# Performance work log

Hardware: AMD Instinct MI355X
Metric: run time of the kernel (lower is better)

## Reference

```python
import jax, jax.numpy as jnp
import numpy as np

D_MODEL = 1024
NHEAD = 16
HEAD_DIM = D_MODEL // NHEAD
B, L = 4, 8192
LN_EPS = 1e-5


def setup_inputs() -> dict:
    key = jax.random.key(0)
    ks = jax.random.split(key, 8)
    s = 1.0 / np.sqrt(D_MODEL)
    return {
        "x": jax.random.normal(ks[0], (B, L, D_MODEL), dtype=jnp.float32),
        "decay": jax.random.uniform(ks[1], (NHEAD,), dtype=jnp.float32, minval=0.8, maxval=0.999),
        "Wq": jax.random.normal(ks[2], (D_MODEL, D_MODEL), dtype=jnp.float32) * s,
        "Wv": jax.random.normal(ks[3], (D_MODEL, D_MODEL), dtype=jnp.float32) * s,
        "Wg": jax.random.normal(ks[4], (D_MODEL, D_MODEL), dtype=jnp.float32) * s,
        "Wo": jax.random.normal(ks[5], (D_MODEL, D_MODEL), dtype=jnp.float32) * s,
        "ln_gamma": jnp.ones((D_MODEL,), dtype=jnp.float32),
        "ln_beta": jnp.zeros((D_MODEL,), dtype=jnp.float32),
    }


def _decay_scan(v, lam):
    # v: (B, L, H, Dh), lam: (H,). s_t = lam * s_{t-1} + v_t, parallel assoc scan over L.
    a = jnp.broadcast_to(lam[None, None, :, None], v.shape)

    def combine(c1, c2):
        a1, b1 = c1
        a2, b2 = c2
        return a1 * a2, b1 * a2 + b2

    _, state = jax.lax.associative_scan(combine, (a, v), axis=1)
    return state


def _layernorm(y, gamma, beta):
    mu = jnp.mean(y, axis=-1, keepdims=True)
    var = jnp.mean(jnp.square(y - mu), axis=-1, keepdims=True)
    return (y - mu) * jax.lax.rsqrt(var + LN_EPS) * gamma + beta


def reference(x, decay, Wq, Wv, Wg, Wo, ln_gamma, ln_beta):
    Bx, Lx, D = x.shape
    q = (x @ Wq.T).reshape(Bx, Lx, NHEAD, HEAD_DIM)
    v = (x @ Wv.T).reshape(Bx, Lx, NHEAD, HEAD_DIM)
    state = _decay_scan(v, decay)                      # (B, L, H, Dh)
    y = (q * state).reshape(Bx, Lx, D)
    y = _layernorm(y, ln_gamma, ln_beta)
    gate = jax.nn.silu(x @ Wg.T)
    y = y * gate
    return y @ Wo.T
```

## Files before the change

kernel.cpp:

```cpp
#include <hip/hip_runtime.h>
#include <cstdint>
#include <cstddef>

typedef unsigned short u16;
typedef __attribute__((ext_vector_type(4))) float f32x4;
typedef __attribute__((ext_vector_type(8))) short s16x8;
typedef __attribute__((ext_vector_type(4))) short s16x4;

#define D_M   1024
#define KDIM  1024
#define BB    4
#define LL    8192
#define MTOT  (BB*LL)
#define CHK   128
#define NCH   (LL/CHK)
#define LN_EPS 1e-5f

static __device__ __forceinline__ float bf2f(u16 u){
  return __uint_as_float(((unsigned)u)<<16);
}
static __device__ __forceinline__ u16 f2bf(float f){
  unsigned u = __float_as_uint(f);
  u += 0x7fffu + ((u>>16)&1u);
  return (u16)(u>>16);
}

__global__ void conv_f2b_k(const float* __restrict__ src, u16* __restrict__ dst, int n4){
  int i = blockIdx.x*blockDim.x + threadIdx.x;
  int stride = gridDim.x*blockDim.x;
  for (; i < n4; i += stride){
    f32x4 f = ((const f32x4*)src)[i];
    s16x4 o;
    o[0]=(short)f2bf(f[0]); o[1]=(short)f2bf(f[1]);
    o[2]=(short)f2bf(f[2]); o[3]=(short)f2bf(f[3]);
    ((s16x4*)dst)[i] = o;
  }
}

template<int F32OUT>
__global__ __launch_bounds__(256,2) void gemm_bt(
    const u16* __restrict__ A,
    const u16* __restrict__ W0, const u16* __restrict__ W1, const u16* __restrict__ W2,
    void* __restrict__ O0, void* __restrict__ O1, void* __restrict__ O2)
{
  __shared__ __align__(16) u16 As[128*64];
  __shared__ __align__(16) u16 Bs[128*64];
  const int mode = blockIdx.z;
  const u16* W = (mode==0)? W0 : ((mode==1)? W1 : W2);
  void* Ov     = (mode==0)? O0 : ((mode==1)? O1 : O2);

  const int tid  = threadIdx.x;
  const int wave = tid>>6, lane = tid&63;
  const int bm = blockIdx.x*128, bn = blockIdx.y*128;

  size_t ga[4], gb[4];
  int lbase[4];
  #pragma unroll
  for (int it=0; it<4; ++it){
    int c    = it*256 + wave*64 + lane;
    int mch  = c>>3;
    int k16  = (c&7) ^ (mch&7);
    ga[it] = (size_t)(bm + mch)*KDIM + (size_t)k16*8;
    gb[it] = (size_t)(bn + mch)*KDIM + (size_t)k16*8;
    lbase[it] = (it*256 + wave*64)*8;
  }

  const int lr = lane&15, lk = lane>>4;
  const int wm = (wave>>1)*64, wn = (wave&1)*64;
  int a_off[4][2], b_off[4][2];
  #pragma unroll
  for (int mi=0; mi<4; ++mi){
    #pragma unroll
    for (int kp=0; kp<2; ++kp){
      int slot = ((kp*4 + lk) ^ (lr&7));
      a_off[mi][kp] = (wm + mi*16 + lr)*128 + slot*16;
      b_off[mi][kp] = (wn + mi*16 + lr)*128 + slot*16;
    }
  }

  const f32x4 fzero = {0.f,0.f,0.f,0.f};
  f32x4 acc[4][4];
  #pragma unroll
  for (int i=0;i<4;i++)
    #pragma unroll
    for (int j=0;j<4;j++)
      acc[i][j] = fzero;

  const char* Asc = (const char*)As;
  const char* Bsc = (const char*)Bs;

  for (int kt=0; kt<KDIM/64; ++kt){
    if (kt) __syncthreads();
    #pragma unroll
    for (int it=0; it<4; ++it){
      __builtin_amdgcn_global_load_lds(
        (const __attribute__((address_space(1))) void*)(A + ga[it] + (size_t)kt*64),
        (__attribute__((address_space(3))) void*)(As + lbase[it]), 16, 0, 0);
      __builtin_amdgcn_global_load_lds(
        (const __attribute__((address_space(1))) void*)(W + gb[it] + (size_t)kt*64),
        (__attribute__((address_space(3))) void*)(Bs + lbase[it]), 16, 0, 0);
    }
    __syncthreads();
    #pragma unroll
    for (int kp=0; kp<2; ++kp){
      s16x8 af[4], bfr[4];
      #pragma unroll
      for (int mi=0; mi<4; ++mi) af[mi]  = *(const s16x8*)(Asc + a_off[mi][kp]);
      #pragma unroll
      for (int ni=0; ni<4; ++ni) bfr[ni] = *(const s16x8*)(Bsc + b_off[ni][kp]);
      #pragma unroll
      for (int mi=0; mi<4; ++mi)
        #pragma unroll
        for (int ni=0; ni<4; ++ni)
          acc[mi][ni] = __builtin_amdgcn_mfma_f32_16x16x32_bf16(af[mi], bfr[ni], acc[mi][ni], 0,0,0);
    }
  }

  const int r0 = bm + wm + (lane>>4)*4;
  const int c0 = bn + wn + (lane&15);
  if (F32OUT){
    float* O = (float*)Ov;
    #pragma unroll
    for (int mi=0; mi<4; ++mi)
      #pragma unroll
      for (int ni=0; ni<4; ++ni)
        #pragma unroll
        for (int r=0;r<4;r++)
          O[(size_t)(r0 + mi*16 + r)*D_M + (c0 + ni*16)] = acc[mi][ni][r];
  } else {
    u16* O = (u16*)Ov;
    const bool do_silu = (mode==2);
    #pragma unroll
    for (int mi=0; mi<4; ++mi)
      #pragma unroll
      for (int ni=0; ni<4; ++ni)
        #pragma unroll
        for (int r=0;r<4;r++){
          float vv = acc[mi][ni][r];
          if (do_silu) vv = vv / (1.f + __expf(-vv));
          O[(size_t)(r0 + mi*16 + r)*D_M + (c0 + ni*16)] = f2bf(vv);
        }
  }
}

__global__ __launch_bounds__(256) void scan1_k(u16* __restrict__ v, float* __restrict__ E,
                                               const float* __restrict__ decay){
  const int c = blockIdx.x, b = blockIdx.y;
  const int d0 = threadIdx.x*4;
  const float lam = decay[d0>>6];
  float s0=0.f,s1=0.f,s2=0.f,s3=0.f;
  u16* p = v + ((size_t)b*LL + (size_t)c*CHK)*D_M + d0;
  for (int i=0;i<CHK;i++){
    s16x4 x = *(const s16x4*)p;
    s0 = fmaf(s0, lam, bf2f((u16)x[0]));
    s1 = fmaf(s1, lam, bf2f((u16)x[1]));
    s2 = fmaf(s2, lam, bf2f((u16)x[2]));
    s3 = fmaf(s3, lam, bf2f((u16)x[3]));
    s16x4 o;
    o[0]=(short)f2bf(s0); o[1]=(short)f2bf(s1);
    o[2]=(short)f2bf(s2); o[3]=(short)f2bf(s3);
    *(s16x4*)p = o;
    p += D_M;
  }
  f32x4 e = {s0,s1,s2,s3};
  *(f32x4*)(E + ((size_t)(b*NCH + c))*D_M + d0) = e;
}

__global__ void scan2_k(const float* __restrict__ E, float* __restrict__ S,
                        const float* __restrict__ decay){
  const int idx = blockIdx.x*blockDim.x + threadIdx.x;
  if (idx >= BB*(D_M/4)) return;
  const int b  = idx / (D_M/4);
  const int d0 = (idx % (D_M/4))*4;
  const float lam  = decay[d0>>6];
  const float lamT = __expf((float)CHK * __logf(lam));
  f32x4 s = {0.f,0.f,0.f,0.f};
  for (int c=0;c<NCH;c++){
    const size_t o = ((size_t)(b*NCH + c))*D_M + d0;
    f32x4 e = *(const f32x4*)(E + o);
    s = s*lamT + e;
    *(f32x4*)(S + o) = s;
  }
}

__global__ __launch_bounds__(256) void fuse_ln_k(
  const u16* __restrict__ qb, const u16* __restrict__ locb, const u16* __restrict__ gateb,
  const float* __restrict__ S, const float* __restrict__ decay,
  const float* __restrict__ gamma, const float* __restrict__ beta,
  u16* __restrict__ yout)
{
  const int token = blockIdx.x;
  const int b  = token >> 13;
  const int t  = token & (LL-1);
  const int c  = t >> 7;
  const int ii = t & (CHK-1);
  const int tid = threadIdx.x;
  const int d0 = tid*4;
  const float lam = decay[d0>>6];
  const float pw  = __expf((float)(ii+1) * __logf(lam));
  f32x4 carry = {0.f,0.f,0.f,0.f};
  if (c > 0) carry = *(const f32x4*)(S + ((size_t)(b*NCH + (c-1)))*D_M + d0);
  const size_t base = (size_t)token*D_M + d0;
  s16x4 q4 = *(const s16x4*)(qb + base);
  s16x4 l4 = *(const s16x4*)(locb + base);
  float y[4];
  #pragma unroll
  for (int j=0;j<4;j++)
    y[j] = bf2f((u16)q4[j]) * (bf2f((u16)l4[j]) + pw*carry[j]);
  float sum = y[0]+y[1]+y[2]+y[3];
  float sq  = y[0]*y[0]+y[1]*y[1]+y[2]*y[2]+y[3]*y[3];
  #pragma unroll
  for (int off=32; off>0; off>>=1){
    sum += __shfl_down(sum, off);
    sq  += __shfl_down(sq , off);
  }
  __shared__ float red[10];
  const int wave = tid>>6, lane = tid&63;
  if (lane==0){ red[wave] = sum; red[4+wave] = sq; }
  __syncthreads();
  if (tid==0){
    float ts = red[0]+red[1]+red[2]+red[3];
    float tq = red[4]+red[5]+red[6]+red[7];
    float mu  = ts * (1.f/(float)D_M);
    float var = tq * (1.f/(float)D_M) - mu*mu;
    red[8] = mu;
    red[9] = rsqrtf(var + LN_EPS);
  }
  __syncthreads();
  const float mu = red[8], rstd = red[9];
  f32x4 gm = *(const f32x4*)(gamma + d0);
  f32x4 bt = *(const f32x4*)(beta  + d0);
  s16x4 g4 = *(const s16x4*)(gateb + base);
  s16x4 o;
  #pragma unroll
  for (int j=0;j<4;j++){
    float nn = (y[j] - mu)*rstd*gm[j] + bt[j];
    nn *= bf2f((u16)g4[j]);
    o[j] = (short)f2bf(nn);
  }
  *(s16x4*)(yout + base) = o;
}

extern "C" void kernel_launch(void* const* d_in, const int* in_sizes, int n_in,
                              void* d_out, int out_size, void* d_ws, size_t ws_size,
                              hipStream_t stream)
{
  const float* x     = (const float*)d_in[0];
  const float* decay = (const float*)d_in[1];
  const float* Wq    = (const float*)d_in[2];
  const float* Wv    = (const float*)d_in[3];
  const float* Wg    = (const float*)d_in[4];
  const float* Wo    = (const float*)d_in[5];
  const float* gamma = (const float*)d_in[6];
  const float* beta  = (const float*)d_in[7];
  float* out = (float*)d_out;

  char* ws = (char*)d_ws;
  size_t off = 0;
  const size_t XB = (size_t)MTOT*D_M*sizeof(u16);
  const size_t WB = (size_t)D_M*KDIM*sizeof(u16);
  const size_t EB = (size_t)BB*NCH*D_M*sizeof(float);
  u16* xb  = (u16*)(ws+off); off += XB;
  u16* Wqb = (u16*)(ws+off); off += WB;
  u16* Wvb = (u16*)(ws+off); off += WB;
  u16* Wgb = (u16*)(ws+off); off += WB;
  u16* Wob = (u16*)(ws+off); off += WB;
  u16* qb  = (u16*)(ws+off); off += XB;
  u16* vb  = (u16*)(ws+off); off += XB;
  u16* gb  = (u16*)(ws+off); off += XB;
  float* E = (float*)(ws+off); off += EB;
  float* S = (float*)(ws+off); off += EB;

  conv_f2b_k<<<dim3(4096), 256, 0, stream>>>(x,  xb,  MTOT*D_M/4);
  conv_f2b_k<<<dim3(512),  256, 0, stream>>>(Wq, Wqb, D_M*KDIM/4);
  conv_f2b_k<<<dim3(512),  256, 0, stream>>>(Wv, Wvb, D_M*KDIM/4);
  conv_f2b_k<<<dim3(512),  256, 0, stream>>>(Wg, Wgb, D_M*KDIM/4);
  conv_f2b_k<<<dim3(512),  256, 0, stream>>>(Wo, Wob, D_M*KDIM/4);

  gemm_bt<0><<<dim3(MTOT/128, D_M/128, 3), 256, 0, stream>>>(xb, Wqb, Wvb, Wgb, qb, vb, gb);

  scan1_k<<<dim3(NCH, BB), 256, 0, stream>>>(vb, E, decay);
  scan2_k<<<dim3(4), 256, 0, stream>>>(E, S, decay);

  fuse_ln_k<<<dim3(MTOT), 256, 0, stream>>>(qb, vb, gb, S, decay, gamma, beta, qb);

  gemm_bt<1><<<dim3(MTOT/128, D_M/128, 1), 256, 0, stream>>>(qb, Wob, Wob, Wob,
                                                             (void*)out, (void*)out, (void*)out);
}
```

Before: 478.3 us.

## Replace GEMM with 256x256 double-buffered 8-wave pipelined kernel, halve scan chunk

Rewrites the bf16 GEMM to use 256x256 tiles with 512 threads, a double-buffered 128KB LDS layout, and an interleaved schedule that issues global-to-LDS loads for later k-tiles between MFMA quadrants, with setprio hints. The aim is to hide memory latency and raise the compute-to-load ratio for the projection and output GEMMs. It also merges the four weight conversions into one launch, shrinks the x-conversion grid, and halves the scan chunk size to 64. In exchange the kernel uses much more LDS and registers, which limits occupancy, and the chunk change doubles the carry array that scan2 walks serially.

Result: faster. 420.2 us (-12.1%).

```diff
diff --git a/kernel.cpp b/kernel.cpp
--- a/kernel.cpp
+++ b/kernel.cpp
@@ -12,8 +12,10 @@
 #define BB    4
 #define LL    8192
 #define MTOT  (BB*LL)
-#define CHK   128
+#define CHK   64
+#define CHK_SH 6
 #define NCH   (LL/CHK)
+#define NT    (KDIM/64)
 #define LN_EPS 1e-5f
 
 static __device__ __forceinline__ float bf2f(u16 u){
@@ -37,109 +39,208 @@
   }
 }
 
+__global__ void conv_w4_k(const float* __restrict__ s0, const float* __restrict__ s1,
+                          const float* __restrict__ s2, const float* __restrict__ s3,
+                          u16* __restrict__ d0, u16* __restrict__ d1,
+                          u16* __restrict__ d2, u16* __restrict__ d3){
+  const float* s; u16* d;
+  switch(blockIdx.y){
+    case 0: s=s0; d=d0; break;
+    case 1: s=s1; d=d1; break;
+    case 2: s=s2; d=d2; break;
+    default: s=s3; d=d3; break;
+  }
+  int i = blockIdx.x*blockDim.x + threadIdx.x;
+  f32x4 f = ((const f32x4*)s)[i];
+  s16x4 o;
+  o[0]=(short)f2bf(f[0]); o[1]=(short)f2bf(f[1]);
+  o[2]=(short)f2bf(f[2]); o[3]=(short)f2bf(f[3]);
+  ((s16x4*)d)[i] = o;
+}
+
 template<int F32OUT>
-__global__ __launch_bounds__(256,2) void gemm_bt(
+__global__ __launch_bounds__(512,2) void gemm256(
     const u16* __restrict__ A,
     const u16* __restrict__ W0, const u16* __restrict__ W1, const u16* __restrict__ W2,
     void* __restrict__ O0, void* __restrict__ O1, void* __restrict__ O2)
 {
-  __shared__ __align__(16) u16 As[128*64];
-  __shared__ __align__(16) u16 Bs[128*64];
+  __shared__ __align__(16) u16 smem[65536];
+
   const int mode = blockIdx.z;
   const u16* W = (mode==0)? W0 : ((mode==1)? W1 : W2);
   void* Ov     = (mode==0)? O0 : ((mode==1)? O1 : O2);
 
   const int tid  = threadIdx.x;
   const int wave = tid>>6, lane = tid&63;
-  const int bm = blockIdx.x*128, bn = blockIdx.y*128;
-
-  size_t ga[4], gb[4];
-  int lbase[4];
-  #pragma unroll
-  for (int it=0; it<4; ++it){
-    int c    = it*256 + wave*64 + lane;
-    int mch  = c>>3;
-    int k16  = (c&7) ^ (mch&7);
-    ga[it] = (size_t)(bm + mch)*KDIM + (size_t)k16*8;
-    gb[it] = (size_t)(bn + mch)*KDIM + (size_t)k16*8;
-    lbase[it] = (it*256 + wave*64)*8;
-  }
+  const int bm = blockIdx.x*256, bn = blockIdx.y*256;
+
+  const int rr = tid>>3;
+  const int kk = (((tid&7) ^ (rr&7)))*8;
+  const int ldw = wave*512;
+
+  #define STAGE(GBASE, LOFF) do {                                                       \
+    const u16* _g = (GBASE) + (size_t)rr*KDIM + kk;                                     \
+    __builtin_amdgcn_global_load_lds(                                                   \
+      (const __attribute__((address_space(1))) void*)(_g),                              \
+      (__attribute__((address_space(3))) void*)(smem + (LOFF) + ldw), 16, 0, 0);        \
+    __builtin_amdgcn_global_load_lds(                                                   \
+      (const __attribute__((address_space(1))) void*)(_g + (size_t)64*KDIM),            \
+      (__attribute__((address_space(3))) void*)(smem + (LOFF) + 4096 + ldw), 16, 0, 0); \
+  } while(0)
 
   const int lr = lane&15, lk = lane>>4;
-  const int wm = (wave>>1)*64, wn = (wave&1)*64;
-  int a_off[4][2], b_off[4][2];
-  #pragma unroll
-  for (int mi=0; mi<4; ++mi){
-    #pragma unroll
-    for (int kp=0; kp<2; ++kp){
-      int slot = ((kp*4 + lk) ^ (lr&7));
-      a_off[mi][kp] = (wm + mi*16 + lr)*128 + slot*16;
-      b_off[mi][kp] = (wn + mi*16 + lr)*128 + slot*16;
-    }
-  }
+  const int wm = wave>>2, wn = wave&3;
+  int aoff[4][2], boff[2][2];
+  #pragma unroll
+  for (int mi=0; mi<4; ++mi)
+    #pragma unroll
+    for (int kp=0; kp<2; ++kp)
+      aoff[mi][kp] = (wm*64 + mi*16 + lr)*64 + (((kp*4+lk) ^ (lr&7)))*8;
+  #pragma unroll
+  for (int ni=0; ni<2; ++ni)
+    #pragma unroll
+    for (int kp=0; kp<2; ++kp)
+      boff[ni][kp] = (wn*32 + ni*16 + lr)*64 + (((kp*4+lk) ^ (lr&7)))*8;
 
   const f32x4 fzero = {0.f,0.f,0.f,0.f};
-  f32x4 acc[4][4];
-  #pragma unroll
-  for (int i=0;i<4;i++)
+  f32x4 acc[8][4];
+  #pragma unroll
+  for (int i=0;i<8;i++)
     #pragma unroll
     for (int j=0;j<4;j++)
       acc[i][j] = fzero;
 
-  const char* Asc = (const char*)As;
-  const char* Bsc = (const char*)Bs;
-
-  for (int kt=0; kt<KDIM/64; ++kt){
-    if (kt) __syncthreads();
-    #pragma unroll
-    for (int it=0; it<4; ++it){
-      __builtin_amdgcn_global_load_lds(
-        (const __attribute__((address_space(1))) void*)(A + ga[it] + (size_t)kt*64),
-        (__attribute__((address_space(3))) void*)(As + lbase[it]), 16, 0, 0);
-      __builtin_amdgcn_global_load_lds(
-        (const __attribute__((address_space(1))) void*)(W + gb[it] + (size_t)kt*64),
-        (__attribute__((address_space(3))) void*)(Bs + lbase[it]), 16, 0, 0);
-    }
-    __syncthreads();
-    #pragma unroll
-    for (int kp=0; kp<2; ++kp){
-      s16x8 af[4], bfr[4];
-      #pragma unroll
-      for (int mi=0; mi<4; ++mi) af[mi]  = *(const s16x8*)(Asc + a_off[mi][kp]);
-      #pragma unroll
-      for (int ni=0; ni<4; ++ni) bfr[ni] = *(const s16x8*)(Bsc + b_off[ni][kp]);
-      #pragma unroll
-      for (int mi=0; mi<4; ++mi)
-        #pragma unroll
-        for (int ni=0; ni<4; ++ni)
-          acc[mi][ni] = __builtin_amdgcn_mfma_f32_16x16x32_bf16(af[mi], bfr[ni], acc[mi][ni], 0,0,0);
-    }
-  }
-
-  const int r0 = bm + wm + (lane>>4)*4;
-  const int c0 = bn + wn + (lane&15);
+  const u16* Abase = A + (size_t)bm*KDIM;
+  const u16* Wbase = W + (size_t)bn*KDIM;
+
+  STAGE(Abase,                    0);
+  STAGE(Wbase,                    32768);
+  STAGE(Wbase + (size_t)128*KDIM, 32768+8192);
+  STAGE(Abase + (size_t)128*KDIM, 8192);
+  STAGE(Abase + 64,                    16384);
+  STAGE(Wbase + 64,                    49152);
+  STAGE(Wbase + (size_t)128*KDIM + 64, 49152+8192);
+  asm volatile("s_waitcnt vmcnt(6)" ::: "memory");
+  __builtin_amdgcn_s_barrier();
+
+  s16x8 afr[4][2], blo[2][2], bhi[2][2];
+
+  for (int kt=0; kt<NT; ++kt){
+    const int cur = kt&1, nxt = cur^1;
+    const int curA = cur*16384;
+    const int curB = 32768 + cur*16384;
+    const int nxtA = nxt*16384;
+    const u16* Ac = smem + curA;
+    const u16* Bc = smem + curB;
+
+    #pragma unroll
+    for (int mi=0; mi<4; ++mi)
+      #pragma unroll
+      for (int kp=0; kp<2; ++kp)
+        afr[mi][kp] = *(const s16x8*)(Ac + aoff[mi][kp]);
+    #pragma unroll
+    for (int ni=0; ni<2; ++ni)
+      #pragma unroll
+      for (int kp=0; kp<2; ++kp)
+        blo[ni][kp] = *(const s16x8*)(Bc + boff[ni][kp]);
+    if (kt+1 < NT) STAGE(Abase + (size_t)128*KDIM + (kt+1)*64, nxtA + 8192);
+    __builtin_amdgcn_s_barrier();
+    __builtin_amdgcn_s_setprio(1);
+    #pragma unroll
+    for (int mi=0; mi<4; ++mi)
+      #pragma unroll
+      for (int ni=0; ni<2; ++ni)
+        #pragma unroll
+        for (int kp=0; kp<2; ++kp)
+          acc[mi][ni] = __builtin_amdgcn_mfma_f32_16x16x32_bf16(afr[mi][kp], blo[ni][kp], acc[mi][ni], 0,0,0);
+    __builtin_amdgcn_s_setprio(0);
+    __builtin_amdgcn_s_barrier();
+
+    #pragma unroll
+    for (int ni=0; ni<2; ++ni)
+      #pragma unroll
+      for (int kp=0; kp<2; ++kp)
+        bhi[ni][kp] = *(const s16x8*)(Bc + 8192 + boff[ni][kp]);
+    if (kt+2 < NT) STAGE(Abase + (kt+2)*64, curA);
+    __builtin_amdgcn_s_barrier();
+    __builtin_amdgcn_s_setprio(1);
+    #pragma unroll
+    for (int mi=0; mi<4; ++mi)
+      #pragma unroll
+      for (int ni=0; ni<2; ++ni)
+        #pragma unroll
+        for (int kp=0; kp<2; ++kp)
+          acc[mi][2+ni] = __builtin_amdgcn_mfma_f32_16x16x32_bf16(afr[mi][kp], bhi[ni][kp], acc[mi][2+ni], 0,0,0);
+    __builtin_amdgcn_s_setprio(0);
+    __builtin_amdgcn_s_barrier();
+
+    #pragma unroll
+    for (int mi=0; mi<4; ++mi)
+      #pragma unroll
+      for (int kp=0; kp<2; ++kp)
+        afr[mi][kp] = *(const s16x8*)(Ac + 8192 + aoff[mi][kp]);
+    if (kt+2 < NT) STAGE(Wbase + (kt+2)*64, curB);
+    __builtin_amdgcn_s_barrier();
+    __builtin_amdgcn_s_setprio(1);
+    #pragma unroll
+    for (int mi=0; mi<4; ++mi)
+      #pragma unroll
+      for (int ni=0; ni<2; ++ni)
+        #pragma unroll
+        for (int kp=0; kp<2; ++kp)
+          acc[4+mi][2+ni] = __builtin_amdgcn_mfma_f32_16x16x32_bf16(afr[mi][kp], bhi[ni][kp], acc[4+mi][2+ni], 0,0,0);
+    __builtin_amdgcn_s_setprio(0);
+    __builtin_amdgcn_s_barrier();
+
+    if (kt+2 < NT) STAGE(Wbase + (size_t)128*KDIM + (kt+2)*64, curB + 8192);
+    __builtin_amdgcn_s_barrier();
+    __builtin_amdgcn_s_setprio(1);
+    #pragma unroll
+    for (int mi=0; mi<4; ++mi)
+      #pragma unroll
+      for (int ni=0; ni<2; ++ni)
+        #pragma unroll
+        for (int kp=0; kp<2; ++kp)
+          acc[4+mi][ni] = __builtin_amdgcn_mfma_f32_16x16x32_bf16(afr[mi][kp], blo[ni][kp], acc[4+mi][ni], 0,0,0);
+    __builtin_amdgcn_s_setprio(0);
+    if (kt < NT-2) { asm volatile("s_waitcnt vmcnt(6)" ::: "memory"); }
+    else           { asm volatile("s_waitcnt vmcnt(0)" ::: "memory"); }
+    __builtin_amdgcn_s_barrier();
+  }
+  #undef STAGE
+
+  const int rq = (lane>>4)*4;
+  const int cl = lane&15;
   if (F32OUT){
     float* O = (float*)Ov;
     #pragma unroll
-    for (int mi=0; mi<4; ++mi)
-      #pragma unroll
-      for (int ni=0; ni<4; ++ni)
+    for (int mi=0; mi<8; ++mi){
+      const int grow = bm + (mi>>2)*128 + wm*64 + (mi&3)*16 + rq;
+      #pragma unroll
+      for (int ni=0; ni<4; ++ni){
+        const int gcol = bn + (ni>>1)*128 + wn*32 + (ni&1)*16 + cl;
         #pragma unroll
         for (int r=0;r<4;r++)
-          O[(size_t)(r0 + mi*16 + r)*D_M + (c0 + ni*16)] = acc[mi][ni][r];
+          O[(size_t)(grow + r)*D_M + gcol] = acc[mi][ni][r];
+      }
+    }
   } else {
     u16* O = (u16*)Ov;
     const bool do_silu = (mode==2);
     #pragma unroll
-    for (int mi=0; mi<4; ++mi)
-      #pragma unroll
-      for (int ni=0; ni<4; ++ni)
+    for (int mi=0; mi<8; ++mi){
+      const int grow = bm + (mi>>2)*128 + wm*64 + (mi&3)*16 + rq;
+      #pragma unroll
+      for (int ni=0; ni<4; ++ni){
+        const int gcol = bn + (ni>>1)*128 + wn*32 + (ni&1)*16 + cl;
         #pragma unroll
         for (int r=0;r<4;r++){
           float vv = acc[mi][ni][r];
           if (do_silu) vv = vv / (1.f + __expf(-vv));
-          O[(size_t)(r0 + mi*16 + r)*D_M + (c0 + ni*16)] = f2bf(vv);
+          O[(size_t)(grow + r)*D_M + gcol] = f2bf(vv);
         }
+      }
+    }
   }
 }
 
@@ -192,7 +293,7 @@
   const int token = blockIdx.x;
   const int b  = token >> 13;
   const int t  = token & (LL-1);
-  const int c  = t >> 7;
+  const int c  = t >> CHK_SH;
   const int ii = t & (CHK-1);
   const int tid = threadIdx.x;
   const int d0 = tid*4;
@@ -271,19 +372,16 @@
   float* E = (float*)(ws+off); off += EB;
   float* S = (float*)(ws+off); off += EB;
 
-  conv_f2b_k<<<dim3(4096), 256, 0, stream>>>(x,  xb,  MTOT*D_M/4);
-  conv_f2b_k<<<dim3(512),  256, 0, stream>>>(Wq, Wqb, D_M*KDIM/4);
-  conv_f2b_k<<<dim3(512),  256, 0, stream>>>(Wv, Wvb, D_M*KDIM/4);
-  conv_f2b_k<<<dim3(512),  256, 0, stream>>>(Wg, Wgb, D_M*KDIM/4);
-  conv_f2b_k<<<dim3(512),  256, 0, stream>>>(Wo, Wob, D_M*KDIM/4);
-
-  gemm_bt<0><<<dim3(MTOT/128, D_M/128, 3), 256, 0, stream>>>(xb, Wqb, Wvb, Wgb, qb, vb, gb);
+  conv_f2b_k<<<dim3(2048), 256, 0, stream>>>(x,  xb,  MTOT*D_M/4);
+  conv_w4_k<<<dim3(1024,4), 256, 0, stream>>>(Wq, Wv, Wg, Wo, Wqb, Wvb, Wgb, Wob);
+
+  gemm256<0><<<dim3(MTOT/256, D_M/256, 3), 512, 0, stream>>>(xb, Wqb, Wvb, Wgb, qb, vb, gb);
 
   scan1_k<<<dim3(NCH, BB), 256, 0, stream>>>(vb, E, decay);
   scan2_k<<<dim3(4), 256, 0, stream>>>(E, S, decay);
 
   fuse_ln_k<<<dim3(MTOT), 256, 0, stream>>>(qb, vb, gb, S, decay, gamma, beta, qb);
 
-  gemm_bt<1><<<dim3(MTOT/128, D_M/128, 1), 256, 0, stream>>>(qb, Wob, Wob, Wob,
+  gemm256<1><<<dim3(MTOT/256, D_M/256, 1), 512, 0, stream>>>(qb, Wob, Wob, Wob,
                                                              (void*)out, (void*)out, (void*)out);
 }
```
